# Performance work log

Hardware: AMD Instinct MI355X
Metric: run time of the kernel (lower is better)

## Reference

```python
import jax, jax.numpy as jnp
import numpy as np

N_SRC, N_DST, E = 50000, 50000, 800000
D_IN, R_DIM, H, D = 256, 64, 8, 32
NEG_SLOPE = 0.2


def setup_inputs() -> dict:
    key = jax.random.key(0)
    ks = jax.random.split(key, 8)
    return {
        "feat_src": jax.random.normal(ks[0], (N_SRC, D_IN), jnp.float32),
        "feat_dst": jax.random.normal(ks[1], (N_DST, D_IN), jnp.float32),
        "src_w": jax.random.normal(ks[2], (D_IN, H * D), jnp.float32) * 0.05,
        "dst_w": jax.random.normal(ks[3], (D_IN, H * D), jnp.float32) * 0.05,
        "rel_emb": jax.random.normal(ks[4], (R_DIM,), jnp.float32),
        "rel_w": jax.random.normal(ks[5], (R_DIM, H * 2 * D), jnp.float32) * 0.05,
        "src_idx": jax.random.randint(ks[6], (E,), 0, N_SRC, jnp.int32),
        "dst_idx": jax.random.randint(ks[7], (E,), 0, N_DST, jnp.int32),
    }


def reference(feat_src, feat_dst, src_w, dst_w, rel_emb, rel_w, src_idx, dst_idx):
    # Node projections (dropout rate = 0 -> identity in eval)
    fs = (feat_src @ src_w).reshape(-1, H, D)   # [N_src, H, D]
    fd = (feat_dst @ dst_w).reshape(-1, H, D)   # [N_dst, H, D]
    rel = (rel_emb @ rel_w).reshape(H, 2 * D)   # [H, 2D]

    # Attention logits per node per head
    e_dst = (fd * rel[:, :D]).sum(-1)           # [N_dst, H]
    e_src = (fs * rel[:, D:]).sum(-1)           # [N_src, H]

    # u_add_v + leaky_relu on edges
    e = jax.nn.leaky_relu(e_src[src_idx] + e_dst[dst_idx], NEG_SLOPE)  # [E, H]

    # edge_softmax: segment softmax grouped by destination node
    m = jax.ops.segment_max(e, dst_idx, num_segments=N_DST)
    m = jnp.where(jnp.isfinite(m), m, jnp.zeros_like(m))
    ex = jnp.exp(e - m[dst_idx])                # [E, H]
    denom = jax.ops.segment_sum(ex, dst_idx, num_segments=N_DST)
    a = ex / denom[dst_idx]                     # [E, H]

    # u_mul_e + sum aggregation
    msg = fs[src_idx] * a[:, :, None]           # [E, H, D]
    out = jax.ops.segment_sum(msg, dst_idx, num_segments=N_DST)
    return jax.nn.relu(out.reshape(N_DST, H * D))
```

## Files before the change

### kernel.cpp

```cpp
#include <hip/hip_runtime.h>
#include <hip/hip_bf16.h>

#define N_SRCN 50000
#define N_DSTN 50000
#define EDGES  800000
#define HEADS  8
#define NEG    0.2f

typedef __attribute__((ext_vector_type(8))) short short8v;
typedef __attribute__((ext_vector_type(4))) float floatx4;

static __device__ __forceinline__ unsigned short f2bf(float f) {
  __hip_bfloat16 h = __float2bfloat16(f);
  unsigned short s;
  __builtin_memcpy(&s, &h, 2);
  return s;
}
static __device__ __forceinline__ float bf2f(unsigned short u) {
  return __uint_as_float(((unsigned)u) << 16);
}

__global__ void bfrag_k(const float* __restrict__ W, short* __restrict__ Bf) {
  int t = blockIdx.x * 256 + threadIdx.x;
  if (t >= 8 * 16 * 64) return;
  int l = t & 63;
  int nb = (t >> 6) & 15;
  int kk = t >> 10;
  int n = nb * 16 + (l & 15);
  int kbase = kk * 32 + ((l >> 4) * 8);
  short* o = Bf + (size_t)t * 8;
#pragma unroll
  for (int j = 0; j < 8; ++j) o[j] = (short)f2bf(W[(size_t)(kbase + j) * 256 + n]);
}

__global__ __launch_bounds__(256) void gemm_fused_k(const float* __restrict__ A,
                                                    const short* __restrict__ Bf,
                                                    const float* __restrict__ rel,
                                                    float* __restrict__ elog,
                                                    unsigned short* __restrict__ fs16,
                                                    int reloff) {
  int rt = blockIdx.x * 4 + (threadIdx.x >> 6);
  if (rt >= 3125) return;
  const int l = threadIdx.x & 63;
  const int r0 = rt * 16;
  const int arow = r0 + (l & 15);
  const int kch = (l >> 4) * 8;

  floatx4 acc[16];
#pragma unroll
  for (int i = 0; i < 16; ++i) acc[i] = (floatx4){0.f, 0.f, 0.f, 0.f};

  for (int kk = 0; kk < 8; ++kk) {
    const float* ap = A + (size_t)arow * 256 + kk * 32 + kch;
    float4 a0 = *(const float4*)ap;
    float4 a1 = *(const float4*)(ap + 4);
    short8v af;
    af[0] = f2bf(a0.x); af[1] = f2bf(a0.y); af[2] = f2bf(a0.z); af[3] = f2bf(a0.w);
    af[4] = f2bf(a1.x); af[5] = f2bf(a1.y); af[6] = f2bf(a1.z); af[7] = f2bf(a1.w);
    const short* bbase = Bf + ((size_t)kk * 16 * 64) * 8 + (size_t)l * 8;
#pragma unroll
    for (int nf = 0; nf < 16; ++nf) {
      short8v bfv = *(const short8v*)(bbase + (size_t)nf * 64 * 8);
      acc[nf] = __builtin_amdgcn_mfma_f32_16x16x32_bf16(af, bfv, acc[nf], 0, 0, 0);
    }
  }
  const int orow = r0 + (l >> 4) * 4;
  const int ocol = l & 15;

  if (fs16) {
#pragma unroll
    for (int nf = 0; nf < 16; ++nf)
#pragma unroll
      for (int r = 0; r < 4; ++r)
        fs16[(size_t)(orow + r) * 256 + nf * 16 + ocol] = f2bf(acc[nf][r]);
  }

  float relv[16];
#pragma unroll
  for (int nf = 0; nf < 16; ++nf)
    relv[nf] = rel[(nf >> 1) * 64 + reloff + (nf & 1) * 16 + ocol];

  float part[8][4];
#pragma unroll
  for (int h = 0; h < 8; ++h)
#pragma unroll
    for (int r = 0; r < 4; ++r)
      part[h][r] = acc[2 * h][r] * relv[2 * h] + acc[2 * h + 1][r] * relv[2 * h + 1];
#pragma unroll
  for (int m = 1; m < 16; m <<= 1)
#pragma unroll
    for (int h = 0; h < 8; ++h)
#pragma unroll
      for (int r = 0; r < 4; ++r)
        part[h][r] += __shfl_xor(part[h][r], m);
#pragma unroll
  for (int h = 0; h < 8; ++h) {
    if (ocol == h) {
#pragma unroll
      for (int r = 0; r < 4; ++r)
        elog[(size_t)(orow + r) * 8 + h] = part[h][r];
    }
  }
}

__global__ void rel_k(const float* __restrict__ rel_emb,
                      const float* __restrict__ rel_w,
                      float* __restrict__ rel) {
  int j = threadIdx.x;
  float s = 0.f;
  for (int r = 0; r < 64; ++r) s += rel_emb[r] * rel_w[r * 512 + j];
  rel[j] = s;
}

__global__ void hist_k(const int* __restrict__ dst, int* __restrict__ counts) {
  int i = blockIdx.x * 256 + threadIdx.x;
  if (i < EDGES) atomicAdd(&counts[dst[i]], 1);
}

__global__ __launch_bounds__(256) void scan1_k(const int* __restrict__ counts,
                                               int* __restrict__ offs,
                                               int* __restrict__ bsum) {
  int i = blockIdx.x * 256 + (int)threadIdx.x;
  int lane = threadIdx.x & 63, w = threadIdx.x >> 6;
  int v = (i < N_DSTN) ? counts[i] : 0;
  int inc = v;
#pragma unroll
  for (int off = 1; off < 64; off <<= 1) {
    int n = __shfl_up(inc, off);
    if (lane >= off) inc += n;
  }
  __shared__ int wt[4];
  if (lane == 63) wt[w] = inc;
  __syncthreads();
  int base = (w > 0 ? wt[0] : 0) + (w > 1 ? wt[1] : 0) + (w > 2 ? wt[2] : 0);
  if (i < N_DSTN) offs[i] = base + inc - v;
  if (threadIdx.x == 255) bsum[blockIdx.x] = base + inc;
}

__global__ __launch_bounds__(256) void scan2_k(int* __restrict__ bsum,
                                               int* __restrict__ bbase) {
  int t = threadIdx.x;
  int lane = t & 63, w = t >> 6;
  int v = (t < 196) ? bsum[t] : 0;
  int inc = v;
#pragma unroll
  for (int off = 1; off < 64; off <<= 1) {
    int n = __shfl_up(inc, off);
    if (lane >= off) inc += n;
  }
  __shared__ int wt[4];
  if (lane == 63) wt[w] = inc;
  __syncthreads();
  int base = (w > 0 ? wt[0] : 0) + (w > 1 ? wt[1] : 0) + (w > 2 ? wt[2] : 0);
  if (t < 196) bbase[t] = base + inc - v;
}

__global__ __launch_bounds__(256) void scan3_k(int* __restrict__ offs,
                                               const int* __restrict__ bbase,
                                               int* __restrict__ cursor) {
  int i = blockIdx.x * 256 + (int)threadIdx.x;
  if (i < N_DSTN) {
    int o = offs[i] + bbase[blockIdx.x];
    offs[i] = o;
    cursor[i] = o;
  }
  if (i == 0) offs[N_DSTN] = EDGES;
}

__global__ void scatter_k(const int* __restrict__ src, const int* __restrict__ dst,
                          int* __restrict__ cursor, int* __restrict__ ssrc) {
  int i = blockIdx.x * 256 + threadIdx.x;
  if (i < EDGES) {
    int p = atomicAdd(&cursor[dst[i]], 1);
    ssrc[p] = src[i];
  }
}

__global__ __launch_bounds__(256) void aggr_k(const unsigned short* __restrict__ fs16,
                                              const float* __restrict__ es,
                                              const float* __restrict__ ed,
                                              const int* __restrict__ offs,
                                              const int* __restrict__ ssrc,
                                              float* __restrict__ out) {
  int wid = (blockIdx.x * 256 + threadIdx.x) >> 6;
  int lane = threadIdx.x & 63;
  if (wid >= N_DSTN) return;
  const int beg = offs[wid], end = offs[wid + 1];
  const int h_a = lane & 7;
  const int le = lane >> 3;
  const int h_c = lane >> 3;
  const float eda = ed[wid * 8 + h_a];
  const float edc = ed[wid * 8 + h_c];

  float mx = -3.4e38f;
  for (int i = beg + le; i < end; i += 8) {
    float v = es[ssrc[i] * 8 + h_a] + eda;
    v = v > 0.f ? v : v * NEG;
    mx = fmaxf(mx, v);
  }
#pragma unroll
  for (int s = 8; s < 64; s <<= 1) mx = fmaxf(mx, __shfl_xor(mx, s));

  float sm = 0.f;
  for (int i = beg + le; i < end; i += 8) {
    float v = es[ssrc[i] * 8 + h_a] + eda;
    v = v > 0.f ? v : v * NEG;
    sm += __expf(v - mx);
  }
#pragma unroll
  for (int s = 8; s < 64; s <<= 1) sm += __shfl_xor(sm, s);

  float m_c = __shfl(mx, h_c);
  float d_c = __shfl(sm, h_c);
  float inv = (end > beg) ? 1.f / d_c : 0.f;

  const int col = lane * 4;
  float4 acc = {0.f, 0.f, 0.f, 0.f};
  for (int i = beg; i < end; ++i) {
    int s = ssrc[i];
    float v = es[s * 8 + h_c] + edc;
    v = v > 0.f ? v : v * NEG;
    float a = __expf(v - m_c) * inv;
    ushort4 fv = *(const ushort4*)&fs16[(size_t)s * 256 + col];
    acc.x += bf2f(fv.x) * a;
    acc.y += bf2f(fv.y) * a;
    acc.z += bf2f(fv.z) * a;
    acc.w += bf2f(fv.w) * a;
  }
  float4 o = {fmaxf(acc.x, 0.f), fmaxf(acc.y, 0.f), fmaxf(acc.z, 0.f),
              fmaxf(acc.w, 0.f)};
  *(float4*)&out[(size_t)wid * 256 + col] = o;
}

extern "C" void kernel_launch(void* const* d_in, const int* in_sizes, int n_in,
                              void* d_out, int out_size, void* d_ws, size_t ws_size,
                              hipStream_t stream) {
  const float* feat_src = (const float*)d_in[0];
  const float* feat_dst = (const float*)d_in[1];
  const float* src_w = (const float*)d_in[2];
  const float* dst_w = (const float*)d_in[3];
  const float* rel_emb = (const float*)d_in[4];
  const float* rel_w = (const float*)d_in[5];
  const int* src_idx = (const int*)d_in[6];
  const int* dst_idx = (const int*)d_in[7];
  float* out = (float*)d_out;

  unsigned short* fs16 = (unsigned short*)d_ws;
  float* rel = (float*)(fs16 + (size_t)N_SRCN * 256);
  float* es = rel + 512;
  float* ed = es + (size_t)N_SRCN * 8;
  int* counts = (int*)(ed + (size_t)N_DSTN * 8);
  int* offs = counts + N_DSTN;
  int* cursor = offs + (N_DSTN + 1);
  int* bsum = cursor + N_DSTN;
  int* bbase = bsum + 256;
  int* ssrc = bbase + 256;
  short* bfS = (short*)(ssrc + EDGES);
  short* bfD = bfS + 65536;

  hipMemsetAsync(counts, 0, N_DSTN * sizeof(int), stream);

  rel_k<<<1, 512, 0, stream>>>(rel_emb, rel_w, rel);
  bfrag_k<<<32, 256, 0, stream>>>(src_w, bfS);
  bfrag_k<<<32, 256, 0, stream>>>(dst_w, bfD);
  gemm_fused_k<<<782, 256, 0, stream>>>(feat_src, bfS, rel, es, fs16, 32);
  gemm_fused_k<<<782, 256, 0, stream>>>(feat_dst, bfD, rel, ed, nullptr, 0);
  hist_k<<<(EDGES + 255) / 256, 256, 0, stream>>>(dst_idx, counts);
  scan1_k<<<196, 256, 0, stream>>>(counts, offs, bsum);
  scan2_k<<<1, 256, 0, stream>>>(bsum, bbase);
  scan3_k<<<196, 256, 0, stream>>>(offs, bbase, cursor);
  scatter_k<<<(EDGES + 255) / 256, 256, 0, stream>>>(src_idx, dst_idx, cursor, ssrc);
  aggr_k<<<(N_DSTN + 3) / 4, 256, 0, stream>>>(fs16, es, ed, offs, ssrc, out);
}
```

Measured before the change: 423.7 us.

## Stage GEMM B fragments in LDS via double buffering; unroll aggregation gathers by four

The fused projection GEMM now copies each k-slice of the pre-packed B fragments into a double-buffered LDS area with global_load_lds. All four waves in a block share that copy instead of each fetching B from global memory, and the next slice is prefetched during the current MFMAs. Out-of-range waves are clamped rather than returned early so they stay in the barriers, which means redundant work and duplicate writes for the last tile. The aggregation loop is unrolled by four so that several independent gathers of logits and features are in flight per destination node.

```diff
diff --git a/kernel.cpp b/kernel.cpp
--- a/kernel.cpp
+++ b/kernel.cpp
@@ -39,31 +39,56 @@
                                                     float* __restrict__ elog,
                                                     unsigned short* __restrict__ fs16,
                                                     int reloff) {
-  int rt = blockIdx.x * 4 + (threadIdx.x >> 6);
-  if (rt >= 3125) return;
-  const int l = threadIdx.x & 63;
+  __shared__ short bsm[2][8192];
+  const int t = threadIdx.x;
+  const int w = t >> 6, l = t & 63;
+  int rt = blockIdx.x * 4 + w;
+  if (rt > 3124) rt = 3124;
   const int r0 = rt * 16;
   const int arow = r0 + (l & 15);
   const int kch = (l >> 4) * 8;
 
+#define STAGE(buf, kk)                                                          \
+  {                                                                             \
+    _Pragma("unroll")                                                           \
+    for (int c = 0; c < 4; ++c) {                                               \
+      const short* g = Bf + (size_t)(kk)*8192 + c * 2048 + w * 512 + l * 8;     \
+      short* d = &bsm[buf][c * 2048 + w * 512];          \
+      __builtin_amdgcn_global_load_lds(                                         \
+          (const __attribute__((address_space(1))) void*)g,                     \
+          (__attribute__((address_space(3))) void*)d, 16, 0, 0);                \
+    }                                                                           \
+  }
+
   floatx4 acc[16];
 #pragma unroll
   for (int i = 0; i < 16; ++i) acc[i] = (floatx4){0.f, 0.f, 0.f, 0.f};
 
+  STAGE(0, 0);
+  asm volatile("s_waitcnt vmcnt(0)" ::: "memory");
+  __builtin_amdgcn_s_barrier();
+
   for (int kk = 0; kk < 8; ++kk) {
+    const int cur = kk & 1;
+    if (kk < 7) STAGE(cur ^ 1, kk + 1);
     const float* ap = A + (size_t)arow * 256 + kk * 32 + kch;
     float4 a0 = *(const float4*)ap;
     float4 a1 = *(const float4*)(ap + 4);
     short8v af;
     af[0] = f2bf(a0.x); af[1] = f2bf(a0.y); af[2] = f2bf(a0.z); af[3] = f2bf(a0.w);
     af[4] = f2bf(a1.x); af[5] = f2bf(a1.y); af[6] = f2bf(a1.z); af[7] = f2bf(a1.w);
-    const short* bbase = Bf + ((size_t)kk * 16 * 64) * 8 + (size_t)l * 8;
 #pragma unroll
     for (int nf = 0; nf < 16; ++nf) {
-      short8v bfv = *(const short8v*)(bbase + (size_t)nf * 64 * 8);
+      short8v bfv = *(const short8v*)&bsm[cur][(nf * 64 + l) * 8];
       acc[nf] = __builtin_amdgcn_mfma_f32_16x16x32_bf16(af, bfv, acc[nf], 0, 0, 0);
     }
-  }
+    if (kk < 7) {
+      asm volatile("s_waitcnt vmcnt(0)" ::: "memory");
+      __builtin_amdgcn_s_barrier();
+    }
+  }
+#undef STAGE
+
   const int orow = r0 + (l >> 4) * 4;
   const int ocol = l & 15;
 
@@ -216,7 +241,33 @@
 
   const int col = lane * 4;
   float4 acc = {0.f, 0.f, 0.f, 0.f};
-  for (int i = beg; i < end; ++i) {
+  int i = beg;
+  for (; i + 4 <= end; i += 4) {
+    int s0 = ssrc[i], s1 = ssrc[i + 1], s2 = ssrc[i + 2], s3 = ssrc[i + 3];
+    float e0 = es[s0 * 8 + h_c], e1 = es[s1 * 8 + h_c];
+    float e2 = es[s2 * 8 + h_c], e3 = es[s3 * 8 + h_c];
+    ushort4 f0 = *(const ushort4*)&fs16[(size_t)s0 * 256 + col];
+    ushort4 f1 = *(const ushort4*)&fs16[(size_t)s1 * 256 + col];
+    ushort4 f2 = *(const ushort4*)&fs16[(size_t)s2 * 256 + col];
+    ushort4 f3 = *(const ushort4*)&fs16[(size_t)s3 * 256 + col];
+    float v0 = e0 + edc; v0 = v0 > 0.f ? v0 : v0 * NEG;
+    float v1 = e1 + edc; v1 = v1 > 0.f ? v1 : v1 * NEG;
+    float v2 = e2 + edc; v2 = v2 > 0.f ? v2 : v2 * NEG;
+    float v3 = e3 + edc; v3 = v3 > 0.f ? v3 : v3 * NEG;
+    float a0 = __expf(v0 - m_c) * inv;
+    float a1 = __expf(v1 - m_c) * inv;
+    float a2 = __expf(v2 - m_c) * inv;
+    float a3 = __expf(v3 - m_c) * inv;
+    acc.x += bf2f(f0.x) * a0; acc.y += bf2f(f0.y) * a0;
+    acc.z += bf2f(f0.z) * a0; acc.w += bf2f(f0.w) * a0;
+    acc.x += bf2f(f1.x) * a1; acc.y += bf2f(f1.y) * a1;
+    acc.z += bf2f(f1.z) * a1; acc.w += bf2f(f1.w) * a1;
+    acc.x += bf2f(f2.x) * a2; acc.y += bf2f(f2.y) * a2;
+    acc.z += bf2f(f2.z) * a2; acc.w += bf2f(f2.w) * a2;
+    acc.x += bf2f(f3.x) * a3; acc.y += bf2f(f3.y) * a3;
+    acc.z += bf2f(f3.z) * a3; acc.w += bf2f(f3.w) * a3;
+  }
+  for (; i < end; ++i) {
     int s = ssrc[i];
     float v = es[s * 8 + h_c] + edc;
     v = v > 0.f ? v : v * NEG;
```

Result: faster. 361.4 us (-14.7%).
